# Optimization experiments

Measured on AMD Instinct MI355X. Metric: run time of the kernel, lower is better.

## Reference

```python
import jax, jax.numpy as jnp
import numpy as np

B, H, O, M = 8192, 1024, 1024, 4

def setup_inputs() -> dict:
    key = jax.random.key(0)
    ks = jax.random.split(key, 8)
    state = jax.random.normal(ks[0], (B, H), dtype=jnp.float32)
    spectral_entropy = jax.random.uniform(ks[1], (B, 1), dtype=jnp.float32)
    curvature = jax.random.normal(ks[2], (B, 1), dtype=jnp.float32)
    # learned params
    modulation_basis = jax.random.normal(ks[3], (M, H, O), dtype=jnp.float32)
    gate_w = jax.random.normal(ks[4], (1, M), dtype=jnp.float32) / jnp.sqrt(1.0)
    gate_b = jax.random.normal(ks[5], (M,), dtype=jnp.float32) * 0.01
    prj_w = jax.random.normal(ks[6], (H, O), dtype=jnp.float32) / jnp.sqrt(H)
    prj_b = jax.random.normal(ks[7], (O,), dtype=jnp.float32) * 0.01
    return {"state": state, "spectral_entropy": spectral_entropy, "curvature": curvature,
            "modulation_basis": modulation_basis, "gate_w": gate_w, "gate_b": gate_b,
            "prj_w": prj_w, "prj_b": prj_b}

def reference(state, spectral_entropy, curvature, modulation_basis, gate_w, gate_b, prj_w, prj_b):
    # softmax gate over modes: [B, M]
    mod_weights = jax.nn.softmax(spectral_entropy @ gate_w + gate_b, axis=-1)
    # Algebraically fused form of einsum('bm,mho->bho') then einsum('bh,bho->bo'):
    # compute per-mode matvec results [B, M, O] (small), then mode-weighted sum.
    mode_out = jnp.einsum('bh,mho->bmo', state, modulation_basis)
    mischief_output = jnp.einsum('bm,bmo->bo', mod_weights, mode_out)
    base_output = state @ prj_w + prj_b
    mix = jax.nn.sigmoid(curvature)  # [B, 1]
    return (1.0 - mix) * base_output + mix * mischief_output
```

## Files before the change

kernel.cpp:

```cpp
#include <hip/hip_runtime.h>
#include <stdint.h>

typedef __attribute__((ext_vector_type(4))) float  float4v;
typedef __attribute__((ext_vector_type(8))) __bf16 bf16x8;
typedef __attribute__((ext_vector_type(8))) unsigned short ushort8;

#define B_DIM 8192
#define H_DIM 1024
#define O_DIM 1024

static __device__ __forceinline__ unsigned short f32_to_bf16(float f) {
  union { float f; unsigned int u; } v; v.f = f;
  unsigned int u = v.u;
  unsigned int r = u + 0x7FFFu + ((u >> 16) & 1u);
  return (unsigned short)(r >> 16);
}

__global__ void prep_inputs(const float* __restrict__ state,
                            const float* __restrict__ basis,
                            const float* __restrict__ prjw,
                            unsigned short* __restrict__ Abf,
                            unsigned short* __restrict__ Wt) {
  __shared__ __align__(16) unsigned short t[64 * 72];
  int bb = blockIdx.x;
  int tid = threadIdx.x;
  if (bb < 1280) {
    int m = bb >> 8, panel = bb & 255;
    int o0 = (panel & 15) * 64, h0 = (panel >> 4) * 64;
    const float* src = (m < 4) ? (basis + (size_t)m * H_DIM * O_DIM) : prjw;
    int r  = tid >> 4;
    int c4 = (tid & 15) * 4;
#pragma unroll
    for (int p = 0; p < 4; ++p) {
      int h = r + p * 16;
      float4v v = *(const float4v*)(src + (size_t)(h0 + h) * O_DIM + o0 + c4);
      t[(c4 + 0) * 72 + h] = f32_to_bf16(v.x);
      t[(c4 + 1) * 72 + h] = f32_to_bf16(v.y);
      t[(c4 + 2) * 72 + h] = f32_to_bf16(v.z);
      t[(c4 + 3) * 72 + h] = f32_to_bf16(v.w);
    }
    __syncthreads();
#pragma unroll
    for (int i = 0; i < 2; ++i) {
      int C = i * 256 + tid;
      int o = C >> 3, cc = C & 7;
      ushort8 val = *(const ushort8*)(t + o * 72 + cc * 8);
      *(ushort8*)(Wt + ((size_t)m * O_DIM + o0 + o) * H_DIM + h0 + cc * 8) = val;
    }
  } else {
    int i = (bb - 1280) * 256 + tid;
    float4v v0 = ((const float4v*)state)[i * 2];
    float4v v1 = ((const float4v*)state)[i * 2 + 1];
    ushort8 o;
    o[0] = f32_to_bf16(v0.x); o[1] = f32_to_bf16(v0.y);
    o[2] = f32_to_bf16(v0.z); o[3] = f32_to_bf16(v0.w);
    o[4] = f32_to_bf16(v1.x); o[5] = f32_to_bf16(v1.y);
    o[6] = f32_to_bf16(v1.z); o[7] = f32_to_bf16(v1.w);
    ((ushort8*)Abf)[i] = o;
  }
}

__global__ __launch_bounds__(256, 2)
void gemm_fused(const unsigned short* __restrict__ A,
                const unsigned short* __restrict__ Wt,
                const float* __restrict__ se, const float* __restrict__ curv,
                const float* __restrict__ gw, const float* __restrict__ gb,
                const float* __restrict__ prjb,
                float* __restrict__ out) {
  __shared__ __align__(16) unsigned char smem[59904];
  float* scf = (float*)(smem + 57344);

  const int tid  = threadIdx.x;
  const int lane = tid & 63;
  const int wave = tid >> 6;
  const int row0 = blockIdx.x * 128;
  const int col0 = blockIdx.y * 64;
  const int wrow = (wave >> 1) * 64;
  const int wcol = (wave & 1) * 32;
  const int q  = lane >> 4;
  const int ln = lane & 15;

  if (tid < 128) {
    int b = row0 + tid;
    float s = se[b];
    float l0 = fmaf(s, gw[0], gb[0]);
    float l1 = fmaf(s, gw[1], gb[1]);
    float l2 = fmaf(s, gw[2], gb[2]);
    float l3 = fmaf(s, gw[3], gb[3]);
    float mx = fmaxf(fmaxf(l0, l1), fmaxf(l2, l3));
    float e0 = __expf(l0 - mx), e1 = __expf(l1 - mx);
    float e2 = __expf(l2 - mx), e3 = __expf(l3 - mx);
    float mix = 1.0f / (1.0f + __expf(-curv[b]));
    float inv = mix / (e0 + e1 + e2 + e3);
    scf[0 * 128 + tid] = e0 * inv;
    scf[1 * 128 + tid] = e1 * inv;
    scf[2 * 128 + tid] = e2 * inv;
    scf[3 * 128 + tid] = e3 * inv;
    scf[4 * 128 + tid] = 1.0f - mix;
  }

  const unsigned short* gA[2];
  unsigned int ldsA[2];
#pragma unroll
  for (int j = 0; j < 2; ++j) {
    int C = (wave * 2 + j) * 64 + lane;
    int row = C >> 2, pos = C & 3;
    int g = pos ^ ((row >> 1) & 3);
    gA[j] = A + (size_t)(row0 + row) * H_DIM + g * 8;
    ldsA[j] = (wave * 2 + j) * 1024;
  }
  const unsigned short* gB[5];
  unsigned int ldsBbase = 8192 + wave * 1024;
  {
    int C = wave * 64 + lane;
    int row = C >> 2, pos = C & 3;
    int g = pos ^ ((row >> 1) & 3);
#pragma unroll
    for (int m = 0; m < 5; ++m)
      gB[m] = Wt + (size_t)m * O_DIM * H_DIM + (size_t)(col0 + row) * H_DIM + g * 8;
  }

  float4v acc[5][4][2];
#pragma unroll
  for (int m = 0; m < 5; ++m)
#pragma unroll
    for (int i = 0; i < 4; ++i)
#pragma unroll
      for (int j = 0; j < 2; ++j)
        acc[m][i][j] = (float4v){0.f, 0.f, 0.f, 0.f};

#define ISSUE_STAGE(s)                                                          \
  do {                                                                          \
    const int _buf = (s) & 1;                                                   \
    const int _k = (s) * 32;                                                    \
    unsigned char* _base = smem + _buf * 28672;                                 \
    _Pragma("unroll")                                                           \
    for (int _j = 0; _j < 2; ++_j)                                              \
      __builtin_amdgcn_global_load_lds(                                         \
          (const __attribute__((address_space(1))) void*)(gA[_j] + _k),         \
          (__attribute__((address_space(3))) void*)(_base + ldsA[_j]), 16, 0, 0);\
    _Pragma("unroll")                                                           \
    for (int _m = 0; _m < 5; ++_m)                                              \
      __builtin_amdgcn_global_load_lds(                                         \
          (const __attribute__((address_space(1))) void*)(gB[_m] + _k),         \
          (__attribute__((address_space(3))) void*)(_base + ldsBbase + _m * 4096),\
          16, 0, 0);                                                            \
  } while (0)

#define COMPUTE_STAGE(s)                                                        \
  do {                                                                          \
    const unsigned short* _sA = (const unsigned short*)(smem + ((s) & 1) * 28672);\
    const unsigned short* _sB = _sA + 4096;                                     \
    bf16x8 _af[4];                                                              \
    _Pragma("unroll")                                                           \
    for (int _t = 0; _t < 4; ++_t) {                                            \
      int _ra = wrow + _t * 16 + ln;                                            \
      int _ps = q ^ ((_ra >> 1) & 3);                                           \
      _af[_t] = *(const bf16x8*)(_sA + _ra * 32 + _ps * 8);                     \
    }                                                                           \
    _Pragma("unroll")                                                           \
    for (int _m = 0; _m < 5; ++_m) {                                            \
      bf16x8 _b0, _b1;                                                          \
      {                                                                         \
        int _rb = wcol + ln;                                                    \
        int _p0 = q ^ ((_rb >> 1) & 3);                                         \
        _b0 = *(const bf16x8*)(_sB + _m * 2048 + _rb * 32 + _p0 * 8);           \
        int _r1 = wcol + 16 + ln;                                               \
        int _p1 = q ^ ((_r1 >> 1) & 3);                                         \
        _b1 = *(const bf16x8*)(_sB + _m * 2048 + _r1 * 32 + _p1 * 8);           \
      }                                                                         \
      _Pragma("unroll")                                                         \
      for (int _ti = 0; _ti < 4; ++_ti) {                                       \
        acc[_m][_ti][0] = __builtin_amdgcn_mfma_f32_16x16x32_bf16(              \
            _af[_ti], _b0, acc[_m][_ti][0], 0, 0, 0);                           \
        acc[_m][_ti][1] = __builtin_amdgcn_mfma_f32_16x16x32_bf16(              \
            _af[_ti], _b1, acc[_m][_ti][1], 0, 0, 0);                           \
      }                                                                         \
    }                                                                           \
  } while (0)

  ISSUE_STAGE(0);
  __syncthreads();
#pragma unroll 2
  for (int s = 0; s < 31; ++s) {
    ISSUE_STAGE(s + 1);
    COMPUTE_STAGE(s);
    __syncthreads();
  }
  COMPUTE_STAGE(31);

  __syncthreads();
  float* fbuf = (float*)smem;
#pragma unroll
  for (int ti = 0; ti < 4; ++ti) {
    int rl = wrow + ti * 16 + q * 4;
#pragma unroll
    for (int tj = 0; tj < 2; ++tj) {
      int cc = wcol + tj * 16 + ln;
#pragma unroll
      for (int r = 0; r < 4; ++r) {
        float v = 0.f;
#pragma unroll
        for (int m = 0; m < 5; ++m)
          v += scf[m * 128 + rl + r] * acc[m][ti][tj][r];
        fbuf[(rl + r) * 68 + cc] = v;
      }
    }
  }
  __syncthreads();
#pragma unroll
  for (int i = 0; i < 8; ++i) {
    int L = i * 256 + tid;
    int row = L >> 4, c4 = L & 15;
    float4v v = *(const float4v*)(fbuf + row * 68 + c4 * 4);
    float cb = scf[4 * 128 + row];
    float4v pb = *(const float4v*)(prjb + col0 + c4 * 4);
    v += cb * pb;
    *(float4v*)(out + (size_t)(row0 + row) * O_DIM + col0 + c4 * 4) = v;
  }
#undef ISSUE_STAGE
#undef COMPUTE_STAGE
}

extern "C" void kernel_launch(void* const* d_in, const int* in_sizes, int n_in,
                              void* d_out, int out_size, void* d_ws, size_t ws_size,
                              hipStream_t stream) {
  const float* state = (const float*)d_in[0];
  const float* se    = (const float*)d_in[1];
  const float* curv  = (const float*)d_in[2];
  const float* basis = (const float*)d_in[3];
  const float* gw    = (const float*)d_in[4];
  const float* gb    = (const float*)d_in[5];
  const float* prjw  = (const float*)d_in[6];
  const float* prjb  = (const float*)d_in[7];
  float* out = (float*)d_out;

  char* ws = (char*)d_ws;
  unsigned short* Abf = (unsigned short*)ws;
  unsigned short* Wt  = (unsigned short*)(ws + (size_t)16 * 1024 * 1024);

  prep_inputs<<<5376, 256, 0, stream>>>(state, basis, prjw, Abf, Wt);
  dim3 gg(B_DIM / 128, O_DIM / 64);
  gemm_fused<<<gg, 256, 0, stream>>>(Abf, Wt, se, curv, gw, gb, prjb, out);
}
```

Before: 187.6 us.

## Use 256-row tiles with a 3-stage LDS pipeline and split load waves

Doubles the GEMM block to 512 threads covering 256 batch rows, so each streamed weight tile is reused across twice as many rows. The two-buffer loop becomes a three-buffer ring using explicit vmcnt waits and raw barriers. Waves 0-3 load the A tiles and waves 4-7 load the five weight slices, and MFMA sections are wrapped in s_setprio. The larger LDS footprint (about 113 KB) likely allows only one block per CU. Hand-tuned wait counts are fragile if the number of loads per wave changes.

Result: faster. 180.6 us (-3.7%).

```diff
diff --git a/kernel.cpp b/kernel.cpp
--- a/kernel.cpp
+++ b/kernel.cpp
@@ -60,27 +60,27 @@
   }
 }
 
-__global__ __launch_bounds__(256, 2)
+__global__ __launch_bounds__(512, 2)
 void gemm_fused(const unsigned short* __restrict__ A,
                 const unsigned short* __restrict__ Wt,
                 const float* __restrict__ se, const float* __restrict__ curv,
                 const float* __restrict__ gw, const float* __restrict__ gb,
                 const float* __restrict__ prjb,
                 float* __restrict__ out) {
-  __shared__ __align__(16) unsigned char smem[59904];
-  float* scf = (float*)(smem + 57344);
+  __shared__ __align__(16) unsigned char smem[115712];
+  float* scf = (float*)(smem + 110592);
 
   const int tid  = threadIdx.x;
   const int lane = tid & 63;
   const int wave = tid >> 6;
-  const int row0 = blockIdx.x * 128;
+  const int row0 = blockIdx.x * 256;
   const int col0 = blockIdx.y * 64;
   const int wrow = (wave >> 1) * 64;
   const int wcol = (wave & 1) * 32;
   const int q  = lane >> 4;
   const int ln = lane & 15;
 
-  if (tid < 128) {
+  if (tid < 256) {
     int b = row0 + tid;
     float s = se[b];
     float l0 = fmaf(s, gw[0], gb[0]);
@@ -92,32 +92,37 @@
     float e2 = __expf(l2 - mx), e3 = __expf(l3 - mx);
     float mix = 1.0f / (1.0f + __expf(-curv[b]));
     float inv = mix / (e0 + e1 + e2 + e3);
-    scf[0 * 128 + tid] = e0 * inv;
-    scf[1 * 128 + tid] = e1 * inv;
-    scf[2 * 128 + tid] = e2 * inv;
-    scf[3 * 128 + tid] = e3 * inv;
-    scf[4 * 128 + tid] = 1.0f - mix;
-  }
-
-  const unsigned short* gA[2];
-  unsigned int ldsA[2];
-#pragma unroll
-  for (int j = 0; j < 2; ++j) {
-    int C = (wave * 2 + j) * 64 + lane;
-    int row = C >> 2, pos = C & 3;
-    int g = pos ^ ((row >> 1) & 3);
-    gA[j] = A + (size_t)(row0 + row) * H_DIM + g * 8;
-    ldsA[j] = (wave * 2 + j) * 1024;
-  }
-  const unsigned short* gB[5];
-  unsigned int ldsBbase = 8192 + wave * 1024;
-  {
-    int C = wave * 64 + lane;
-    int row = C >> 2, pos = C & 3;
-    int g = pos ^ ((row >> 1) & 3);
-#pragma unroll
-    for (int m = 0; m < 5; ++m)
-      gB[m] = Wt + (size_t)m * O_DIM * H_DIM + (size_t)(col0 + row) * H_DIM + g * 8;
+    scf[0 * 256 + tid] = e0 * inv;
+    scf[1 * 256 + tid] = e1 * inv;
+    scf[2 * 256 + tid] = e2 * inv;
+    scf[3 * 256 + tid] = e3 * inv;
+    scf[4 * 256 + tid] = 1.0f - mix;
+  }
+
+  const unsigned short* gsrc[5];
+  unsigned int ldsoff[5];
+  if (wave < 4) {
+#pragma unroll
+    for (int j = 0; j < 4; ++j) {
+      int c = wave * 4 + j;
+      int row = c * 16 + (lane >> 2);
+      int pos = lane & 3;
+      int g = pos ^ ((row >> 1) & 3);
+      gsrc[j] = A + (size_t)(row0 + row) * H_DIM + g * 8;
+      ldsoff[j] = c * 1024;
+    }
+    gsrc[4] = gsrc[0]; ldsoff[4] = ldsoff[0];
+  } else {
+#pragma unroll
+    for (int j = 0; j < 5; ++j) {
+      int c = (wave - 4) * 5 + j;
+      int m = c >> 2;
+      int r = (c & 3) * 16 + (lane >> 2);
+      int pos = lane & 3;
+      int g = pos ^ ((r >> 1) & 3);
+      gsrc[j] = Wt + (size_t)m * O_DIM * H_DIM + (size_t)(col0 + r) * H_DIM + g * 8;
+      ldsoff[j] = 16384 + c * 1024;
+    }
   }
 
   float4v acc[5][4][2];
@@ -129,28 +134,42 @@
       for (int j = 0; j < 2; ++j)
         acc[m][i][j] = (float4v){0.f, 0.f, 0.f, 0.f};
 
-#define ISSUE_STAGE(s)                                                          \
-  do {                                                                          \
-    const int _buf = (s) & 1;                                                   \
-    const int _k = (s) * 32;                                                    \
-    unsigned char* _base = smem + _buf * 28672;                                 \
-    _Pragma("unroll")                                                           \
-    for (int _j = 0; _j < 2; ++_j)                                              \
-      __builtin_amdgcn_global_load_lds(                                         \
-          (const __attribute__((address_space(1))) void*)(gA[_j] + _k),         \
-          (__attribute__((address_space(3))) void*)(_base + ldsA[_j]), 16, 0, 0);\
-    _Pragma("unroll")                                                           \
-    for (int _m = 0; _m < 5; ++_m)                                              \
-      __builtin_amdgcn_global_load_lds(                                         \
-          (const __attribute__((address_space(1))) void*)(gB[_m] + _k),         \
-          (__attribute__((address_space(3))) void*)(_base + ldsBbase + _m * 4096),\
-          16, 0, 0);                                                            \
-  } while (0)
-
-#define COMPUTE_STAGE(s)                                                        \
-  do {                                                                          \
-    const unsigned short* _sA = (const unsigned short*)(smem + ((s) & 1) * 28672);\
-    const unsigned short* _sB = _sA + 4096;                                     \
+#define ISSUE_STAGE(koff, boff)                                                 \
+  do {                                                                          \
+    if (wave < 4) {                                                             \
+      _Pragma("unroll")                                                         \
+      for (int _j = 0; _j < 4; ++_j)                                            \
+        __builtin_amdgcn_global_load_lds(                                       \
+            (const __attribute__((address_space(1))) void*)(gsrc[_j] + (koff)), \
+            (__attribute__((address_space(3))) void*)(smem + (boff) + ldsoff[_j]),\
+            16, 0, 0);                                                          \
+    } else {                                                                    \
+      _Pragma("unroll")                                                         \
+      for (int _j = 0; _j < 5; ++_j)                                            \
+        __builtin_amdgcn_global_load_lds(                                       \
+            (const __attribute__((address_space(1))) void*)(gsrc[_j] + (koff)), \
+            (__attribute__((address_space(3))) void*)(smem + (boff) + ldsoff[_j]),\
+            16, 0, 0);                                                          \
+    }                                                                           \
+  } while (0)
+
+#define WAITV_STEADY                                                            \
+  do {                                                                          \
+    if (wave < 4) asm volatile("s_waitcnt vmcnt(8)" ::: "memory");              \
+    else          asm volatile("s_waitcnt vmcnt(10)" ::: "memory");             \
+  } while (0)
+#define WAITV_ONE                                                               \
+  do {                                                                          \
+    if (wave < 4) asm volatile("s_waitcnt vmcnt(4)" ::: "memory");              \
+    else          asm volatile("s_waitcnt vmcnt(5)" ::: "memory");              \
+  } while (0)
+#define WAITV_ZERO asm volatile("s_waitcnt vmcnt(0)" ::: "memory")
+
+#define COMPUTE_STAGE(boff)                                                     \
+  do {                                                                          \
+    const unsigned short* _sA = (const unsigned short*)(smem + (boff));         \
+    const unsigned short* _sB = _sA + 8192;                                     \
+    __builtin_amdgcn_s_setprio(1);                                              \
     bf16x8 _af[4];                                                              \
     _Pragma("unroll")                                                           \
     for (int _t = 0; _t < 4; ++_t) {                                            \
@@ -177,17 +196,36 @@
             _af[_ti], _b1, acc[_m][_ti][1], 0, 0, 0);                           \
       }                                                                         \
     }                                                                           \
-  } while (0)
-
-  ISSUE_STAGE(0);
-  __syncthreads();
-#pragma unroll 2
-  for (int s = 0; s < 31; ++s) {
-    ISSUE_STAGE(s + 1);
-    COMPUTE_STAGE(s);
-    __syncthreads();
-  }
-  COMPUTE_STAGE(31);
+    __builtin_amdgcn_s_setprio(0);                                              \
+  } while (0)
+
+  ISSUE_STAGE(0, 0u);
+  ISSUE_STAGE(32, 36864u);
+  ISSUE_STAGE(64, 73728u);
+  asm volatile("s_waitcnt lgkmcnt(0)" ::: "memory");
+  WAITV_STEADY;
+  __builtin_amdgcn_s_barrier();
+
+  unsigned int boff = 0u;
+  int kk = 96;
+  for (int s = 0; s < 29; ++s) {
+    COMPUTE_STAGE(boff);
+    __builtin_amdgcn_s_barrier();
+    ISSUE_STAGE(kk, boff);
+    WAITV_STEADY;
+    __builtin_amdgcn_s_barrier();
+    kk += 32;
+    boff = (boff == 73728u) ? 0u : boff + 36864u;
+  }
+  COMPUTE_STAGE(boff);
+  WAITV_ONE;
+  __builtin_amdgcn_s_barrier();
+  boff = (boff == 73728u) ? 0u : boff + 36864u;
+  COMPUTE_STAGE(boff);
+  WAITV_ZERO;
+  __builtin_amdgcn_s_barrier();
+  boff = (boff == 73728u) ? 0u : boff + 36864u;
+  COMPUTE_STAGE(boff);
 
   __syncthreads();
   float* fbuf = (float*)smem;
@@ -202,7 +240,7 @@
         float v = 0.f;
 #pragma unroll
         for (int m = 0; m < 5; ++m)
-          v += scf[m * 128 + rl + r] * acc[m][ti][tj][r];
+          v += scf[m * 256 + rl + r] * acc[m][ti][tj][r];
         fbuf[(rl + r) * 68 + cc] = v;
       }
     }
@@ -210,15 +248,18 @@
   __syncthreads();
 #pragma unroll
   for (int i = 0; i < 8; ++i) {
-    int L = i * 256 + tid;
+    int L = i * 512 + tid;
     int row = L >> 4, c4 = L & 15;
     float4v v = *(const float4v*)(fbuf + row * 68 + c4 * 4);
-    float cb = scf[4 * 128 + row];
+    float cb = scf[4 * 256 + row];
     float4v pb = *(const float4v*)(prjb + col0 + c4 * 4);
     v += cb * pb;
     *(float4v*)(out + (size_t)(row0 + row) * O_DIM + col0 + c4 * 4) = v;
   }
 #undef ISSUE_STAGE
+#undef WAITV_STEADY
+#undef WAITV_ONE
+#undef WAITV_ZERO
 #undef COMPUTE_STAGE
 }
 
@@ -240,6 +281,6 @@
   unsigned short* Wt  = (unsigned short*)(ws + (size_t)16 * 1024 * 1024);
 
   prep_inputs<<<5376, 256, 0, stream>>>(state, basis, prjw, Abf, Wt);
-  dim3 gg(B_DIM / 128, O_DIM / 64);
-  gemm_fused<<<gg, 256, 0, stream>>>(Abf, Wt, se, curv, gw, gb, prjb, out);
-}
+  dim3 gg(B_DIM / 256, O_DIM / 64);
+  gemm_fused<<<gg, 512, 0, stream>>>(Abf, Wt, se, curv, gw, gb, prjb, out);
+}
```

## Load MFMA operands directly from global into registers, dropping LDS staging

Applied to the files above, without the earlier changes.

Replaces the LDS double-buffered global_load_lds pipeline with per-wave direct global-to-register loads of A and B fragments. Two register sets are ping-ponged so the next k-slice loads while the current one feeds MFMAs, and s_setprio raises wave priority during MFMA bursts. This removes the per-stage barriers and LDS traffic, but each wave now fetches its own fragments, so data shared by waves in the block is fetched redundantly through the caches with less coalesced access. Register pressure also rises sharply at launch bounds 256,2. Shared memory shrinks to the epilogue buffer only.

Result: slower. 513.1 us (+173.5%).

```diff
diff --git a/kernel.cpp b/kernel.cpp
--- a/kernel.cpp
+++ b/kernel.cpp
@@ -67,8 +67,8 @@
                 const float* __restrict__ gw, const float* __restrict__ gb,
                 const float* __restrict__ prjb,
                 float* __restrict__ out) {
-  __shared__ __align__(16) unsigned char smem[59904];
-  float* scf = (float*)(smem + 57344);
+  __shared__ __align__(16) unsigned char smem[39424];
+  float* scf = (float*)(smem + 36864);
 
   const int tid  = threadIdx.x;
   const int lane = tid & 63;
@@ -99,26 +99,17 @@
     scf[4 * 128 + tid] = 1.0f - mix;
   }
 
-  const unsigned short* gA[2];
-  unsigned int ldsA[2];
-#pragma unroll
-  for (int j = 0; j < 2; ++j) {
-    int C = (wave * 2 + j) * 64 + lane;
-    int row = C >> 2, pos = C & 3;
-    int g = pos ^ ((row >> 1) & 3);
-    gA[j] = A + (size_t)(row0 + row) * H_DIM + g * 8;
-    ldsA[j] = (wave * 2 + j) * 1024;
-  }
-  const unsigned short* gB[5];
-  unsigned int ldsBbase = 8192 + wave * 1024;
-  {
-    int C = wave * 64 + lane;
-    int row = C >> 2, pos = C & 3;
-    int g = pos ^ ((row >> 1) & 3);
-#pragma unroll
-    for (int m = 0; m < 5; ++m)
-      gB[m] = Wt + (size_t)m * O_DIM * H_DIM + (size_t)(col0 + row) * H_DIM + g * 8;
-  }
+  const unsigned short* pA[4];
+#pragma unroll
+  for (int t = 0; t < 4; ++t)
+    pA[t] = A + (size_t)(row0 + wrow + 16 * t + ln) * H_DIM + 8 * q;
+  const unsigned short* pB[5][2];
+#pragma unroll
+  for (int m = 0; m < 5; ++m)
+#pragma unroll
+    for (int j = 0; j < 2; ++j)
+      pB[m][j] = Wt + (size_t)m * O_DIM * H_DIM +
+                 (size_t)(col0 + wcol + 16 * j + ln) * H_DIM + 8 * q;
 
   float4v acc[5][4][2];
 #pragma unroll
@@ -129,65 +120,54 @@
       for (int j = 0; j < 2; ++j)
         acc[m][i][j] = (float4v){0.f, 0.f, 0.f, 0.f};
 
-#define ISSUE_STAGE(s)                                                          \
+  bf16x8 ae[4], beF[5][2], ao[4], boF[5][2];
+
+#define LOADSET(aF, bF, koff)                                                   \
   do {                                                                          \
-    const int _buf = (s) & 1;                                                   \
-    const int _k = (s) * 32;                                                    \
-    unsigned char* _base = smem + _buf * 28672;                                 \
     _Pragma("unroll")                                                           \
-    for (int _j = 0; _j < 2; ++_j)                                              \
-      __builtin_amdgcn_global_load_lds(                                         \
-          (const __attribute__((address_space(1))) void*)(gA[_j] + _k),         \
-          (__attribute__((address_space(3))) void*)(_base + ldsA[_j]), 16, 0, 0);\
+    for (int _t = 0; _t < 4; ++_t)                                              \
+      aF[_t] = *(const bf16x8*)(pA[_t] + (koff));                               \
+    _Pragma("unroll")                                                           \
+    for (int _m = 0; _m < 5; ++_m) {                                            \
+      bF[_m][0] = *(const bf16x8*)(pB[_m][0] + (koff));                         \
+      bF[_m][1] = *(const bf16x8*)(pB[_m][1] + (koff));                         \
+    }                                                                           \
+  } while (0)
+
+#define MFMASET(aF, bF)                                                         \
+  do {                                                                          \
+    __builtin_amdgcn_s_setprio(1);                                              \
     _Pragma("unroll")                                                           \
     for (int _m = 0; _m < 5; ++_m)                                              \
-      __builtin_amdgcn_global_load_lds(                                         \
-          (const __attribute__((address_space(1))) void*)(gB[_m] + _k),         \
-          (__attribute__((address_space(3))) void*)(_base + ldsBbase + _m * 4096),\
-          16, 0, 0);                                                            \
+      _Pragma("unroll")                                                         \
+      for (int _t = 0; _t < 4; ++_t) {                                          \
+        acc[_m][_t][0] = __builtin_amdgcn_mfma_f32_16x16x32_bf16(               \
+            aF[_t], bF[_m][0], acc[_m][_t][0], 0, 0, 0);                        \
+        acc[_m][_t][1] = __builtin_amdgcn_mfma_f32_16x16x32_bf16(               \
+            aF[_t], bF[_m][1], acc[_m][_t][1], 0, 0, 0);                        \
+      }                                                                         \
+    __builtin_amdgcn_s_setprio(0);                                              \
   } while (0)
 
-#define COMPUTE_STAGE(s)                                                        \
+#define BUMP64                                                                  \
   do {                                                                          \
-    const unsigned short* _sA = (const unsigned short*)(smem + ((s) & 1) * 28672);\
-    const unsigned short* _sB = _sA + 4096;                                     \
-    bf16x8 _af[4];                                                              \
-    _Pragma("unroll")                                                           \
-    for (int _t = 0; _t < 4; ++_t) {                                            \
-      int _ra = wrow + _t * 16 + ln;                                            \
-      int _ps = q ^ ((_ra >> 1) & 3);                                           \
-      _af[_t] = *(const bf16x8*)(_sA + _ra * 32 + _ps * 8);                     \
-    }                                                                           \
-    _Pragma("unroll")                                                           \
-    for (int _m = 0; _m < 5; ++_m) {                                            \
-      bf16x8 _b0, _b1;                                                          \
-      {                                                                         \
-        int _rb = wcol + ln;                                                    \
-        int _p0 = q ^ ((_rb >> 1) & 3);                                         \
-        _b0 = *(const bf16x8*)(_sB + _m * 2048 + _rb * 32 + _p0 * 8);           \
-        int _r1 = wcol + 16 + ln;                                               \
-        int _p1 = q ^ ((_r1 >> 1) & 3);                                         \
-        _b1 = *(const bf16x8*)(_sB + _m * 2048 + _r1 * 32 + _p1 * 8);           \
-      }                                                                         \
-      _Pragma("unroll")                                                         \
-      for (int _ti = 0; _ti < 4; ++_ti) {                                       \
-        acc[_m][_ti][0] = __builtin_amdgcn_mfma_f32_16x16x32_bf16(              \
-            _af[_ti], _b0, acc[_m][_ti][0], 0, 0, 0);                           \
-        acc[_m][_ti][1] = __builtin_amdgcn_mfma_f32_16x16x32_bf16(              \
-            _af[_ti], _b1, acc[_m][_ti][1], 0, 0, 0);                           \
-      }                                                                         \
+    _Pragma("unroll") for (int _t = 0; _t < 4; ++_t) pA[_t] += 64;              \
+    _Pragma("unroll") for (int _m = 0; _m < 5; ++_m) {                          \
+      pB[_m][0] += 64; pB[_m][1] += 64;                                         \
     }                                                                           \
   } while (0)
 
-  ISSUE_STAGE(0);
-  __syncthreads();
-#pragma unroll 2
-  for (int s = 0; s < 31; ++s) {
-    ISSUE_STAGE(s + 1);
-    COMPUTE_STAGE(s);
-    __syncthreads();
-  }
-  COMPUTE_STAGE(31);
+  LOADSET(ae, beF, 0);
+  for (int it = 0; it < 15; ++it) {
+    LOADSET(ao, boF, 32);
+    MFMASET(ae, beF);
+    LOADSET(ae, beF, 64);
+    MFMASET(ao, boF);
+    BUMP64;
+  }
+  LOADSET(ao, boF, 32);
+  MFMASET(ae, beF);
+  MFMASET(ao, boF);
 
   __syncthreads();
   float* fbuf = (float*)smem;
@@ -218,8 +198,9 @@
     v += cb * pb;
     *(float4v*)(out + (size_t)(row0 + row) * O_DIM + col0 + c4 * 4) = v;
   }
-#undef ISSUE_STAGE
-#undef COMPUTE_STAGE
+#undef LOADSET
+#undef MFMASET
+#undef BUMP64
 }
 
 extern "C" void kernel_launch(void* const* d_in, const int* in_sizes, int n_in,
```
